# Optimization experiments

Hardware: AMD Instinct MI355X
Metric: run time of the kernel (lower is better)

## Reference

```python
import jax, jax.numpy as jnp
import numpy as np

B, T, D = 2, 2048, 2048
H, KV = 16, 4
HD = D // H  # 128
ROPE_BASE = 10000.0


def _rope(t):
    # t: [B, h, T, HD]; faithful to torch apply_rope (even/odd split, concat halves)
    pos = jnp.arange(T, dtype=t.dtype)
    inv_freq = 1.0 / (ROPE_BASE ** (jnp.arange(0, HD, 2, dtype=t.dtype) / HD))
    ang = jnp.einsum('t,f->tf', pos, inv_freq)  # [T, HD/2]
    sin = jnp.sin(ang)[None, None]
    cos = jnp.cos(ang)[None, None]
    t1, t2 = t[..., ::2], t[..., 1::2]
    return jnp.concatenate([t1 * cos - t2 * sin, t1 * sin + t2 * cos], axis=-1)


def setup_inputs() -> dict:
    key = jax.random.key(0)
    kx, kq, kk, kv, ko = jax.random.split(key, 5)
    x = jax.random.normal(kx, (B, T, D), dtype=jnp.float32)
    s = 0.02
    Wq = jax.random.normal(kq, (D, D), dtype=jnp.float32) * s
    Wk = jax.random.normal(kk, (D, KV * HD), dtype=jnp.float32) * s
    Wv = jax.random.normal(kv, (D, KV * HD), dtype=jnp.float32) * s
    Wo = jax.random.normal(ko, (D, D), dtype=jnp.float32) * s
    return {"x": x, "Wq": Wq, "Wk": Wk, "Wv": Wv, "Wo": Wo}


def reference(x, Wq, Wk, Wv, Wo):
    # projections (nn.Linear, no bias)
    q = (x @ Wq).reshape(B, T, H, HD).transpose(0, 2, 1, 3)    # [B,H,T,HD]
    k = (x @ Wk).reshape(B, T, KV, HD).transpose(0, 2, 1, 3)   # [B,KV,T,HD]
    v = (x @ Wv).reshape(B, T, KV, HD).transpose(0, 2, 1, 3)
    q = _rope(q)
    k = _rope(k)
    # GQA: repeat_interleave kv heads to full head count
    g = H // KV
    k = jnp.repeat(k, g, axis=1)
    v = jnp.repeat(v, g, axis=1)
    # causal SDPA, default scale 1/sqrt(head_dim)
    scale = 1.0 / jnp.sqrt(jnp.array(HD, dtype=x.dtype))
    scores = jnp.einsum('bhqd,bhkd->bhqk', q, k) * scale
    mask = jnp.tril(jnp.ones((T, T), dtype=bool))
    scores = jnp.where(mask, scores, jnp.finfo(scores.dtype).min)
    attn = jax.nn.softmax(scores, axis=-1)
    out = jnp.einsum('bhqk,bhkd->bhqd', attn, v)               # [B,H,T,HD]
    out = out.transpose(0, 2, 1, 3).reshape(B, T, D)
    return out @ Wo
```

## Files before the change

kernel.cpp:

```cpp
#include <hip/hip_runtime.h>
#include <math.h>

#define BB 2
#define TT 2048
#define DD 2048
#define HH 16
#define KVHN 4
#define HDIM 128
#define NKV 3072

typedef unsigned short u16;
typedef unsigned int u32;
typedef __bf16 bf16x8 __attribute__((ext_vector_type(8)));
typedef float  f32x4  __attribute__((ext_vector_type(4)));

#define AS1 __attribute__((address_space(1)))
#define AS3 __attribute__((address_space(3)))

__device__ __forceinline__ void dma16(const u16* g, u16* l) {
  __builtin_amdgcn_global_load_lds((const AS1 u32*)g, (AS3 u32*)l, 16, 0, 0);
}

__device__ __forceinline__ u16 f2bf(float f) {
  u32 u = __float_as_uint(f);
  u32 r = (u + 0x7FFFu + ((u >> 16) & 1u)) >> 16;
  return (u16)r;
}
__device__ __forceinline__ float bf2f(u32 h) { return __uint_as_float(h << 16); }

__device__ __forceinline__ u32 pack2(float a, float b) {
  union { __bf16 h[2]; u32 u; } cv;
  cv.h[0] = (__bf16)a; cv.h[1] = (__bf16)b;
  return cv.u;
}

__global__ __launch_bounds__(256) void castf2b(const float* __restrict__ in,
                                               u16* __restrict__ out) {
  size_t i4 = (size_t)blockIdx.x * 256 + threadIdx.x;
  float4 v = *(const float4*)(in + i4 * 4);
  ushort4 o;
  o.x = f2bf(v.x); o.y = f2bf(v.y); o.z = f2bf(v.z); o.w = f2bf(v.w);
  *(ushort4*)(out + i4 * 4) = o;
}

__global__ __launch_bounds__(256) void tcast(const float* __restrict__ W,
                                             u16* __restrict__ WT,
                                             int K, int N) {
  __shared__ float tile[32][33];
  const int n0 = blockIdx.x * 32, k0 = blockIdx.y * 32;
  const int r = threadIdx.x >> 3;
  const int c4 = (threadIdx.x & 7) * 4;
  float4 v = *(const float4*)(W + (size_t)(k0 + r) * N + n0 + c4);
  tile[r][c4 + 0] = v.x; tile[r][c4 + 1] = v.y;
  tile[r][c4 + 2] = v.z; tile[r][c4 + 3] = v.w;
  __syncthreads();
  ushort4 o;
  o.x = f2bf(tile[c4 + 0][r]); o.y = f2bf(tile[c4 + 1][r]);
  o.z = f2bf(tile[c4 + 2][r]); o.w = f2bf(tile[c4 + 3][r]);
  *(ushort4*)(WT + (size_t)(n0 + r) * K + k0 + c4) = o;
}

template <int OUT_BF16>
__global__ __launch_bounds__(512) void gemm8p(const u16* __restrict__ A,
                                              const u16* __restrict__ BT,
                                              void* __restrict__ Cv,
                                              int N, int K) {
  __shared__ u16 lds[3 * 24576];
  const int t = threadIdx.x;
  const int l = t & 63, w = t >> 6;
  const int lm = l & 15, quad = l >> 4;
  const int wm = w & 1, wn = w >> 1;
  const int m0 = blockIdx.y * 128, n0 = blockIdx.x * 256;
  const int wu = __builtin_amdgcn_readfirstlane(w);

  const u16* srcA[2]; int dstA[2];
  const u16* srcB[4]; int dstB[4];
  #pragma unroll
  for (int i = 0; i < 2; ++i) {
    int p0 = (wu * 2 + i) * 64, p = p0 + l;
    int row = p >> 3, c = (p & 7) ^ (row & 7);
    srcA[i] = A + (size_t)(m0 + row) * K + c * 8;
    dstA[i] = p0 * 8;
  }
  #pragma unroll
  for (int i = 0; i < 4; ++i) {
    int p0 = (wu * 4 + i) * 64, p = p0 + l;
    int row = p >> 3, c = (p & 7) ^ (row & 7);
    srcB[i] = BT + (size_t)(n0 + row) * K + c * 8;
    dstB[i] = 8192 + p0 * 8;
  }

  f32x4 acc[4][4];
  #pragma unroll
  for (int i = 0; i < 4; ++i)
    #pragma unroll
    for (int j = 0; j < 4; ++j) acc[i][j] = (f32x4){0.f, 0.f, 0.f, 0.f};

  auto stage = [&](int bsel) {
    u16* buf = &lds[bsel * 24576];
    #pragma unroll
    for (int i = 0; i < 2; ++i) { dma16(srcA[i], buf + dstA[i]); srcA[i] += 64; }
    #pragma unroll
    for (int i = 0; i < 4; ++i) { dma16(srcB[i], buf + dstB[i]); srcB[i] += 64; }
  };

  stage(0); stage(1); stage(2);

  const int NT = K >> 6;
  int bsel = 0;
  const int xorc = lm & 7;
  for (int tI = 0; tI < NT; ++tI) {
    if (tI + 2 < NT)      asm volatile("s_waitcnt vmcnt(12)" ::: "memory");
    else if (tI + 1 < NT) asm volatile("s_waitcnt vmcnt(6)" ::: "memory");
    else                  asm volatile("s_waitcnt vmcnt(0)" ::: "memory");
    asm volatile("s_barrier" ::: "memory");

    const u16* Ab = &lds[bsel * 24576];
    const u16* Bb = Ab + 8192;
    bf16x8 a[2][4], b[2][4];
    #pragma unroll
    for (int ks = 0; ks < 2; ++ks) {
      int ch = ((ks * 4 + quad) ^ xorc) * 8;
      #pragma unroll
      for (int i = 0; i < 4; ++i)
        a[ks][i] = *(const bf16x8*)&Ab[(wm * 64 + i * 16 + lm) * 64 + ch];
      #pragma unroll
      for (int j = 0; j < 4; ++j)
        b[ks][j] = *(const bf16x8*)&Bb[(wn * 64 + j * 16 + lm) * 64 + ch];
    }
    __builtin_amdgcn_s_setprio(1);
    #pragma unroll
    for (int ks = 0; ks < 2; ++ks)
      #pragma unroll
      for (int i = 0; i < 4; ++i)
        #pragma unroll
        for (int j = 0; j < 4; ++j)
          acc[i][j] = __builtin_amdgcn_mfma_f32_16x16x32_bf16(a[ks][i], b[ks][j], acc[i][j], 0, 0, 0);
    __builtin_amdgcn_s_setprio(0);
    asm volatile("s_barrier" ::: "memory");
    if (tI + 3 < NT) stage(bsel);
    bsel = (bsel == 2) ? 0 : bsel + 1;
  }

  #pragma unroll
  for (int i = 0; i < 4; ++i) {
    #pragma unroll
    for (int r = 0; r < 4; ++r) {
      size_t gr = (size_t)(m0 + wm * 64 + i * 16 + quad * 4 + r);
      #pragma unroll
      for (int j = 0; j < 4; ++j) {
        int gc = n0 + wn * 64 + j * 16 + lm;
        if (OUT_BF16) ((u16*)Cv)[gr * N + gc] = f2bf(acc[i][j][r]);
        else          ((float*)Cv)[gr * N + gc] = acc[i][j][r];
      }
    }
  }
}

__global__ __launch_bounds__(256) void rope2(u16* p) {
  const int row = blockIdx.x;
  const int pos = row & (TT - 1);
  u16* base = p + (size_t)row * NKV;
  float e0[5], e1[5];
  #pragma unroll
  for (int i = 0; i < 5; ++i) {
    int item = threadIdx.x + i * 256;
    int h20 = item >> 6, f = item & 63;
    int col = (h20 < 16) ? h20 * 128 : 2048 + (h20 - 16) * 128;
    u32 u = *(const u32*)(base + col + 2 * f);
    e0[i] = bf2f(u & 0xffffu);
    e1[i] = bf2f(u >> 16);
  }
  __syncthreads();
  #pragma unroll
  for (int i = 0; i < 5; ++i) {
    int item = threadIdx.x + i * 256;
    int h20 = item >> 6, f = item & 63;
    int col = (h20 < 16) ? h20 * 128 : 2048 + (h20 - 16) * 128;
    float sc = (h20 < 16) ? 0.08838834764831845f : 1.0f;
    float inv = exp2f((float)f * -0.20762050593046898f);
    float ang = (float)pos * inv;
    float sn, cs;
    sincosf(ang, &sn, &cs);
    base[col + f]      = f2bf((e0[i] * cs - e1[i] * sn) * sc);
    base[col + 64 + f] = f2bf((e0[i] * sn + e1[i] * cs) * sc);
  }
}

__global__ __launch_bounds__(256) void vtrans(const u16* __restrict__ QKV,
                                              u16* __restrict__ Vt) {
  __shared__ u16 tl[64][72];
  const int t0 = blockIdx.x * 64;
  const int y  = blockIdx.y;
  const int b  = blockIdx.z;
  #pragma unroll
  for (int i = 0; i < 2; ++i) {
    int idx = threadIdx.x + i * 256;
    int r = idx >> 3, c = (idx & 7) * 8;
    *(uint4*)&tl[r][c] =
        *(const uint4*)(QKV + (size_t)(b * TT + t0 + r) * NKV + 2560 + y * 64 + c);
  }
  __syncthreads();
  const int vh = y >> 1;
  #pragma unroll
  for (int i = 0; i < 2; ++i) {
    int idx = threadIdx.x + i * 256;
    int dr = idx >> 3, tc = (idx & 7) * 8;
    u16 tmp[8];
    #pragma unroll
    for (int j = 0; j < 8; ++j) tmp[j] = tl[tc + j][dr];
    int dloc = (y & 1) * 64 + dr;
    *(uint4*)(Vt + (size_t)((b * KVHN + vh) * HDIM + dloc) * TT + t0 + tc) =
        *(const uint4*)tmp;
  }
}

__global__ __launch_bounds__(256, 4) void attn4(const u16* __restrict__ QKV,
                                                const u16* __restrict__ Vt,
                                                u16* __restrict__ Ob) {
  __shared__ u16 KsA[32 * 128], KsB[32 * 128];
  __shared__ u16 VsA[64 * 64], VsB[64 * 64];
  __shared__ u16 Pw[4 * 512];
  const int t = threadIdx.x;
  const int l = t & 63, w = t >> 6;
  const int lm = l & 15, quad = l >> 4;
  const int h = blockIdx.y, b = blockIdx.z;
  const int qbase = (blockIdx.x + (blockIdx.y & 7)) & 31;
  const int qt = (blockIdx.y & 8) ? (31 - qbase) : qbase;
  const int kvh = h >> 2;
  const int q0 = qt * 64;
  const int last = 2 * qt + 1;
  const int wu = __builtin_amdgcn_readfirstlane(w);
  u16* pwv = &Pw[w * 512];
  constexpr float L2E = 1.4426950408889634f;

  bf16x8 qf[4];
  {
    size_t r0 = (size_t)(b * TT + q0 + w * 16 + lm) * NKV + h * HDIM;
    #pragma unroll
    for (int ks = 0; ks < 4; ++ks)
      qf[ks] = *(const bf16x8*)(QKV + r0 + ks * 32 + quad * 8);
  }

  f32x4 o[8];
  #pragma unroll
  for (int i = 0; i < 8; ++i) o[i] = (f32x4){0.f, 0.f, 0.f, 0.f};
  float m_ = -1e30f, l_ = 0.f;

  const u16 *kg[2], *vg[2];
  int koff[2], voff[2];
  #pragma unroll
  for (int i = 0; i < 2; ++i) {
    int p0 = (wu * 2 + i) * 64, p = p0 + l;
    int krow = p >> 4, kcp = p & 15, kcl = kcp ^ (krow & 15);
    kg[i] = QKV + (size_t)(b * TT + krow) * NKV + 2048 + kvh * HDIM + kcl * 8;
    koff[i] = p0 * 8;
    int vrow = p >> 3, vphys = p & 7, vcl = vphys ^ (vrow & 7);
    int vd = vrow + (vcl >> 2) * 64, vtch = vcl & 3;
    vg[i] = Vt + (size_t)((b * KVHN + kvh) * HDIM + vd) * TT + vtch * 8;
    voff[i] = p0 * 8;
  }

  #pragma unroll
  for (int i = 0; i < 2; ++i) {
    dma16(kg[i], KsA + koff[i]);
    dma16(vg[i], VsA + voff[i]);
    kg[i] += 32 * NKV;
    vg[i] += 32;
  }

  const int qrow = q0 + w * 16 + lm;

  auto body = [&](int kt, const u16* kcur, const u16* vcur, u16* knx, u16* vnx) {
    __syncthreads();
    const bool pf = kt < last;
    if (pf) {
      #pragma unroll
      for (int i = 0; i < 2; ++i) dma16(vg[i], vnx + voff[i]);
    }

    f32x4 s[2];
    s[0] = (f32x4){0.f, 0.f, 0.f, 0.f};
    s[1] = (f32x4){0.f, 0.f, 0.f, 0.f};
    __builtin_amdgcn_s_setprio(1);
    #pragma unroll
    for (int ks = 0; ks < 4; ++ks) {
      #pragma unroll
      for (int mt = 0; mt < 2; ++mt) {
        bf16x8 kb = *(const bf16x8*)&kcur[(mt * 16 + lm) * 128 + (((ks * 4 + quad) ^ lm) * 8)];
        s[mt] = __builtin_amdgcn_mfma_f32_16x16x32_bf16(kb, qf[ks], s[mt], 0, 0, 0);
      }
    }
    __builtin_amdgcn_s_setprio(0);
    if (pf) {
      #pragma unroll
      for (int i = 0; i < 2; ++i) {
        dma16(kg[i], knx + koff[i]);
        kg[i] += 32 * NKV;
        vg[i] += 32;
      }
    }

    if (kt >= 2 * qt) {
      #pragma unroll
      for (int mt = 0; mt < 2; ++mt)
        #pragma unroll
        for (int r = 0; r < 4; ++r) {
          int kv = kt * 32 + mt * 16 + quad * 4 + r;
          if (kv > qrow) s[mt][r] = -1e30f;
        }
    }

    float mx = -1e30f;
    #pragma unroll
    for (int mt = 0; mt < 2; ++mt)
      #pragma unroll
      for (int r = 0; r < 4; ++r) mx = fmaxf(mx, s[mt][r]);
    mx = fmaxf(mx, __shfl_xor(mx, 16));
    mx = fmaxf(mx, __shfl_xor(mx, 32));
    bool upd = mx > m_ + 8.f;
    float mn = upd ? mx : m_;
    float al = upd ? exp2f((m_ - mn) * L2E) : 1.f;
    m_ = mn;
    float sum = 0.f;
    #pragma unroll
    for (int mt = 0; mt < 2; ++mt)
      #pragma unroll
      for (int r = 0; r < 4; ++r) {
        float pv = exp2f((s[mt][r] - mn) * L2E);
        s[mt][r] = pv;
        sum += pv;
      }
    sum += __shfl_xor(sum, 16);
    sum += __shfl_xor(sum, 32);
    l_ = l_ * al + sum;

    #pragma unroll
    for (int mt = 0; mt < 2; ++mt) {
      u32 p01 = pack2(s[mt][0], s[mt][1]);
      u32 p23 = pack2(s[mt][2], s[mt][3]);
      int c = mt * 2 + (quad >> 1);
      int addr = (lm >> 1) * 64 + ((lm & 1) * 4 + (c ^ ((lm >> 1) & 3))) * 8 + (quad & 1) * 4;
      uint2 uv; uv.x = p01; uv.y = p23;
      *(uint2*)&pwv[addr] = uv;
    }
    if (__any(upd)) {
      #pragma unroll
      for (int i = 0; i < 8; ++i)
        #pragma unroll
        for (int r = 0; r < 4; ++r) o[i][r] *= al;
    }

    int paddr = (lm >> 1) * 64 + ((lm & 1) * 4 + (quad ^ ((lm >> 1) & 3))) * 8;
    bf16x8 pb = *(const bf16x8*)&pwv[paddr];
    __builtin_amdgcn_s_setprio(1);
    #pragma unroll
    for (int mt2 = 0; mt2 < 8; ++mt2) {
      int vrow = (mt2 & 3) * 16 + lm;
      int vphys = ((mt2 >> 2) * 4 + quad) ^ (vrow & 7);
      bf16x8 vb = *(const bf16x8*)&vcur[vrow * 64 + vphys * 8];
      o[mt2] = __builtin_amdgcn_mfma_f32_16x16x32_bf16(vb, pb, o[mt2], 0, 0, 0);
    }
    __builtin_amdgcn_s_setprio(0);
  };

  for (int kt = 0; kt <= last; ++kt) {
    if ((kt & 1) == 0) body(kt, KsA, VsA, KsB, VsB);
    else               body(kt, KsB, VsB, KsA, VsA);
  }

  __syncthreads();
  u16* esc = ((w & 2) ? KsB : KsA) + (w & 1) * 2048;
  float inv = 1.f / l_;
  #pragma unroll
  for (int mt2 = 0; mt2 < 8; ++mt2) {
    u32 a0 = pack2(o[mt2][0] * inv, o[mt2][1] * inv);
    u32 a1 = pack2(o[mt2][2] * inv, o[mt2][3] * inv);
    int phys = (mt2 * 2 + (quad >> 1)) ^ (lm & 7);
    int addr = lm * 128 + phys * 8 + (quad & 1) * 4;
    uint2 uv; uv.x = a0; uv.y = a1;
    *(uint2*)&esc[addr] = uv;
  }
  #pragma unroll
  for (int i = 0; i < 4; ++i) {
    int p = i * 64 + l;
    int row = p >> 4, cl = p & 15;
    int cph = cl ^ (row & 7);
    uint4 val = *(const uint4*)&esc[row * 128 + cph * 8];
    *(uint4*)(Ob + (size_t)(b * TT + q0 + w * 16 + row) * DD + h * HDIM + cl * 8) = val;
  }
}

extern "C" void kernel_launch(void* const* d_in, const int* in_sizes, int n_in,
                              void* d_out, int out_size, void* d_ws, size_t ws_size,
                              hipStream_t stream) {
  const float* x  = (const float*)d_in[0];
  const float* Wq = (const float*)d_in[1];
  const float* Wk = (const float*)d_in[2];
  const float* Wv = (const float*)d_in[3];
  const float* Wo = (const float*)d_in[4];
  float* out = (float*)d_out;

  u16* xb    = (u16*)d_ws;
  u16* WqkvT = xb + 8388608;
  u16* WoT   = xb + 14680064;
  u16* Vt    = WqkvT;
  u16* Ob    = xb;
  u16* QKVb  = (u16*)d_out;

  dim3 blk(256);
  castf2b<<<8192, blk, 0, stream>>>(x, xb);
  tcast<<<dim3(64, 64), blk, 0, stream>>>(Wq, WqkvT, DD, DD);
  tcast<<<dim3(16, 64), blk, 0, stream>>>(Wk, WqkvT + (size_t)2048 * DD, DD, 512);
  tcast<<<dim3(16, 64), blk, 0, stream>>>(Wv, WqkvT + (size_t)2560 * DD, DD, 512);
  tcast<<<dim3(64, 64), blk, 0, stream>>>(Wo, WoT, DD, DD);

  gemm8p<1><<<dim3(NKV / 256, 32), dim3(512), 0, stream>>>(xb, WqkvT, QKVb, NKV, DD);
  rope2<<<BB * TT, blk, 0, stream>>>(QKVb);
  vtrans<<<dim3(32, 8, BB), blk, 0, stream>>>(QKVb, Vt);
  attn4<<<dim3(32, HH, BB), blk, 0, stream>>>(QKVb, Vt, Ob);
  gemm8p<0><<<dim3(DD / 256, 32), dim3(512), 0, stream>>>(Ob, WoT, out, DD, DD);
}
```

Baseline: 326.4 us.

## Halve GEMM K-tile to 32 and triple-buffer attention K/V loads

The GEMM now stages 32-wide K tiles instead of 64, with the swizzle and vmcnt thresholds adjusted. This halves LDS per block, which may allow more resident blocks, but doubles the number of barrier iterations. The attention kernel replaces its double buffer with a three-stage K/V ring that uses explicit vmcnt waits and two barriers per iteration, and its launch bound drops to 3 waves. The aim is deeper prefetch to hide load latency, at the cost of more LDS and lower target occupancy.

```diff
diff --git a/kernel.cpp b/kernel.cpp
--- a/kernel.cpp
+++ b/kernel.cpp
@@ -65,7 +65,7 @@
                                               const u16* __restrict__ BT,
                                               void* __restrict__ Cv,
                                               int N, int K) {
-  __shared__ u16 lds[3 * 24576];
+  __shared__ u16 lds[3 * 12288];
   const int t = threadIdx.x;
   const int l = t & 63, w = t >> 6;
   const int lm = l & 15, quad = l >> 4;
@@ -73,21 +73,20 @@
   const int m0 = blockIdx.y * 128, n0 = blockIdx.x * 256;
   const int wu = __builtin_amdgcn_readfirstlane(w);
 
-  const u16* srcA[2]; int dstA[2];
-  const u16* srcB[4]; int dstB[4];
+  const u16* srcA; int dstA;
+  const u16* srcB[2]; int dstB[2];
+  {
+    int p0 = wu * 64, p = p0 + l;
+    int row = p >> 2, c = (p & 3) ^ (row & 3);
+    srcA = A + (size_t)(m0 + row) * K + c * 8;
+    dstA = p0 * 8;
+  }
   #pragma unroll
   for (int i = 0; i < 2; ++i) {
     int p0 = (wu * 2 + i) * 64, p = p0 + l;
-    int row = p >> 3, c = (p & 7) ^ (row & 7);
-    srcA[i] = A + (size_t)(m0 + row) * K + c * 8;
-    dstA[i] = p0 * 8;
-  }
-  #pragma unroll
-  for (int i = 0; i < 4; ++i) {
-    int p0 = (wu * 4 + i) * 64, p = p0 + l;
-    int row = p >> 3, c = (p & 7) ^ (row & 7);
+    int row = p >> 2, c = (p & 3) ^ (row & 3);
     srcB[i] = BT + (size_t)(n0 + row) * K + c * 8;
-    dstB[i] = 8192 + p0 * 8;
+    dstB[i] = 4096 + p0 * 8;
   }
 
   f32x4 acc[4][4];
@@ -97,45 +96,39 @@
     for (int j = 0; j < 4; ++j) acc[i][j] = (f32x4){0.f, 0.f, 0.f, 0.f};
 
   auto stage = [&](int bsel) {
-    u16* buf = &lds[bsel * 24576];
-    #pragma unroll
-    for (int i = 0; i < 2; ++i) { dma16(srcA[i], buf + dstA[i]); srcA[i] += 64; }
-    #pragma unroll
-    for (int i = 0; i < 4; ++i) { dma16(srcB[i], buf + dstB[i]); srcB[i] += 64; }
+    u16* buf = &lds[bsel * 12288];
+    dma16(srcA, buf + dstA); srcA += 32;
+    #pragma unroll
+    for (int i = 0; i < 2; ++i) { dma16(srcB[i], buf + dstB[i]); srcB[i] += 32; }
   };
 
   stage(0); stage(1); stage(2);
 
-  const int NT = K >> 6;
+  const int NT = K >> 5;
   int bsel = 0;
-  const int xorc = lm & 7;
+  const int xc = lm & 3;
   for (int tI = 0; tI < NT; ++tI) {
-    if (tI + 2 < NT)      asm volatile("s_waitcnt vmcnt(12)" ::: "memory");
-    else if (tI + 1 < NT) asm volatile("s_waitcnt vmcnt(6)" ::: "memory");
+    if (tI + 2 < NT)      asm volatile("s_waitcnt vmcnt(6)" ::: "memory");
+    else if (tI + 1 < NT) asm volatile("s_waitcnt vmcnt(3)" ::: "memory");
     else                  asm volatile("s_waitcnt vmcnt(0)" ::: "memory");
     asm volatile("s_barrier" ::: "memory");
 
-    const u16* Ab = &lds[bsel * 24576];
-    const u16* Bb = Ab + 8192;
-    bf16x8 a[2][4], b[2][4];
-    #pragma unroll
-    for (int ks = 0; ks < 2; ++ks) {
-      int ch = ((ks * 4 + quad) ^ xorc) * 8;
-      #pragma unroll
-      for (int i = 0; i < 4; ++i)
-        a[ks][i] = *(const bf16x8*)&Ab[(wm * 64 + i * 16 + lm) * 64 + ch];
+    const u16* Ab = &lds[bsel * 12288];
+    const u16* Bb = Ab + 4096;
+    const int ch = (quad ^ xc) * 8;
+    bf16x8 a[4], b[4];
+    #pragma unroll
+    for (int i = 0; i < 4; ++i)
+      a[i] = *(const bf16x8*)&Ab[(wm * 64 + i * 16 + lm) * 32 + ch];
+    #pragma unroll
+    for (int j = 0; j < 4; ++j)
+      b[j] = *(const bf16x8*)&Bb[(wn * 64 + j * 16 + lm) * 32 + ch];
+    __builtin_amdgcn_s_setprio(1);
+    #pragma unroll
+    for (int i = 0; i < 4; ++i)
       #pragma unroll
       for (int j = 0; j < 4; ++j)
-        b[ks][j] = *(const bf16x8*)&Bb[(wn * 64 + j * 16 + lm) * 64 + ch];
-    }
-    __builtin_amdgcn_s_setprio(1);
-    #pragma unroll
-    for (int ks = 0; ks < 2; ++ks)
-      #pragma unroll
-      for (int i = 0; i < 4; ++i)
-        #pragma unroll
-        for (int j = 0; j < 4; ++j)
-          acc[i][j] = __builtin_amdgcn_mfma_f32_16x16x32_bf16(a[ks][i], b[ks][j], acc[i][j], 0, 0, 0);
+        acc[i][j] = __builtin_amdgcn_mfma_f32_16x16x32_bf16(a[i], b[j], acc[i][j], 0, 0, 0);
     __builtin_amdgcn_s_setprio(0);
     asm volatile("s_barrier" ::: "memory");
     if (tI + 3 < NT) stage(bsel);
@@ -215,11 +208,11 @@
   }
 }
 
-__global__ __launch_bounds__(256, 4) void attn4(const u16* __restrict__ QKV,
+__global__ __launch_bounds__(256, 3) void attn5(const u16* __restrict__ QKV,
                                                 const u16* __restrict__ Vt,
                                                 u16* __restrict__ Ob) {
-  __shared__ u16 KsA[32 * 128], KsB[32 * 128];
-  __shared__ u16 VsA[64 * 64], VsB[64 * 64];
+  __shared__ u16 Ks[3 * 4096];
+  __shared__ u16 Vs[3 * 4096];
   __shared__ u16 Pw[4 * 512];
   const int t = threadIdx.x;
   const int l = t & 63, w = t >> 6;
@@ -261,23 +254,31 @@
     voff[i] = p0 * 8;
   }
 
-  #pragma unroll
-  for (int i = 0; i < 2; ++i) {
-    dma16(kg[i], KsA + koff[i]);
-    dma16(vg[i], VsA + voff[i]);
-    kg[i] += 32 * NKV;
-    vg[i] += 32;
-  }
+  auto stageKV = [&](int bsel) {
+    u16* kd = Ks + bsel * 4096;
+    u16* vd = Vs + bsel * 4096;
+    #pragma unroll
+    for (int i = 0; i < 2; ++i) {
+      dma16(kg[i], kd + koff[i]);  kg[i] += 32 * NKV;
+      dma16(vg[i], vd + voff[i]);  vg[i] += 32;
+    }
+  };
+
+  stageKV(0);
+  if (1 <= last) stageKV(1);
+  if (2 <= last) stageKV(2);
 
   const int qrow = q0 + w * 16 + lm;
 
-  auto body = [&](int kt, const u16* kcur, const u16* vcur, u16* knx, u16* vnx) {
-    __syncthreads();
-    const bool pf = kt < last;
-    if (pf) {
-      #pragma unroll
-      for (int i = 0; i < 2; ++i) dma16(vg[i], vnx + voff[i]);
-    }
+  int bs = 0;
+  for (int kt = 0; kt <= last; ++kt) {
+    if (kt + 2 <= last)      asm volatile("s_waitcnt vmcnt(8)" ::: "memory");
+    else if (kt + 1 <= last) asm volatile("s_waitcnt vmcnt(4)" ::: "memory");
+    else                     asm volatile("s_waitcnt vmcnt(0)" ::: "memory");
+    asm volatile("s_barrier" ::: "memory");
+
+    const u16* kcur = Ks + bs * 4096;
+    const u16* vcur = Vs + bs * 4096;
 
     f32x4 s[2];
     s[0] = (f32x4){0.f, 0.f, 0.f, 0.f};
@@ -292,14 +293,6 @@
       }
     }
     __builtin_amdgcn_s_setprio(0);
-    if (pf) {
-      #pragma unroll
-      for (int i = 0; i < 2; ++i) {
-        dma16(kg[i], knx + koff[i]);
-        kg[i] += 32 * NKV;
-        vg[i] += 32;
-      }
-    }
 
     if (kt >= 2 * qt) {
       #pragma unroll
@@ -362,15 +355,14 @@
       o[mt2] = __builtin_amdgcn_mfma_f32_16x16x32_bf16(vb, pb, o[mt2], 0, 0, 0);
     }
     __builtin_amdgcn_s_setprio(0);
-  };
-
-  for (int kt = 0; kt <= last; ++kt) {
-    if ((kt & 1) == 0) body(kt, KsA, VsA, KsB, VsB);
-    else               body(kt, KsB, VsB, KsA, VsA);
+
+    asm volatile("s_barrier" ::: "memory");
+    if (kt + 3 <= last) stageKV(bs);
+    bs = (bs == 2) ? 0 : bs + 1;
   }
 
   __syncthreads();
-  u16* esc = ((w & 2) ? KsB : KsA) + (w & 1) * 2048;
+  u16* esc = Ks + (w >> 1) * 4096 + (w & 1) * 2048;
   float inv = 1.f / l_;
   #pragma unroll
   for (int mt2 = 0; mt2 < 8; ++mt2) {
@@ -418,6 +410,6 @@
   gemm8p<1><<<dim3(NKV / 256, 32), dim3(512), 0, stream>>>(xb, WqkvT, QKVb, NKV, DD);
   rope2<<<BB * TT, blk, 0, stream>>>(QKVb);
   vtrans<<<dim3(32, 8, BB), blk, 0, stream>>>(QKVb, Vt);
-  attn4<<<dim3(32, HH, BB), blk, 0, stream>>>(QKVb, Vt, Ob);
+  attn5<<<dim3(32, HH, BB), blk, 0, stream>>>(QKVb, Vt, Ob);
   gemm8p<0><<<dim3(DD / 256, 32), dim3(512), 0, stream>>>(Ob, WoT, out, DD, DD);
 }
```

After: 341.3 us. +4.6%, slower.

## Interleave next-tile DMA with MFMA phases in GEMM, prefetch depth two

Applied to the files above, without the earlier changes.

Restructures the GEMM main loop so the global-to-LDS loads for the tile two steps ahead are issued in two halves between the k-sub-step LDS reads, each followed by a barrier and its MFMA batch. Previously a whole tile was staged only after all MFMAs finished. Prefetch depth drops from three tiles in flight to two, with matching waitcnt values. Lane-to-address mapping for the DMA becomes thread-contiguous. The aim is to spread memory issue across compute and cut post-compute stalls, at the cost of extra barriers per tile and less latency hiding.

```diff
diff --git a/kernel.cpp b/kernel.cpp
--- a/kernel.cpp
+++ b/kernel.cpp
@@ -61,7 +61,7 @@
 }
 
 template <int OUT_BF16>
-__global__ __launch_bounds__(512) void gemm8p(const u16* __restrict__ A,
+__global__ __launch_bounds__(512) void gemm4p(const u16* __restrict__ A,
                                               const u16* __restrict__ BT,
                                               void* __restrict__ Cv,
                                               int N, int K) {
@@ -72,22 +72,23 @@
   const int wm = w & 1, wn = w >> 1;
   const int m0 = blockIdx.y * 128, n0 = blockIdx.x * 256;
   const int wu = __builtin_amdgcn_readfirstlane(w);
+  const int tid = wu * 64 + l;
 
   const u16* srcA[2]; int dstA[2];
   const u16* srcB[4]; int dstB[4];
   #pragma unroll
   for (int i = 0; i < 2; ++i) {
-    int p0 = (wu * 2 + i) * 64, p = p0 + l;
+    int p = tid + i * 512;
     int row = p >> 3, c = (p & 7) ^ (row & 7);
     srcA[i] = A + (size_t)(m0 + row) * K + c * 8;
-    dstA[i] = p0 * 8;
+    dstA[i] = p * 8;
   }
   #pragma unroll
   for (int i = 0; i < 4; ++i) {
-    int p0 = (wu * 4 + i) * 64, p = p0 + l;
+    int p = tid + i * 512;
     int row = p >> 3, c = (p & 7) ^ (row & 7);
     srcB[i] = BT + (size_t)(n0 + row) * K + c * 8;
-    dstB[i] = 8192 + p0 * 8;
+    dstB[i] = 8192 + p * 8;
   }
 
   f32x4 acc[4][4];
@@ -96,7 +97,7 @@
     #pragma unroll
     for (int j = 0; j < 4; ++j) acc[i][j] = (f32x4){0.f, 0.f, 0.f, 0.f};
 
-  auto stage = [&](int bsel) {
+  auto stage_full = [&](int bsel) {
     u16* buf = &lds[bsel * 24576];
     #pragma unroll
     for (int i = 0; i < 2; ++i) { dma16(srcA[i], buf + dstA[i]); srcA[i] += 64; }
@@ -104,42 +105,53 @@
     for (int i = 0; i < 4; ++i) { dma16(srcB[i], buf + dstB[i]); srcB[i] += 64; }
   };
 
-  stage(0); stage(1); stage(2);
+  stage_full(0); stage_full(1);
 
   const int NT = K >> 6;
-  int bsel = 0;
-  const int xorc = lm & 7;
   for (int tI = 0; tI < NT; ++tI) {
-    if (tI + 2 < NT)      asm volatile("s_waitcnt vmcnt(12)" ::: "memory");
-    else if (tI + 1 < NT) asm volatile("s_waitcnt vmcnt(6)" ::: "memory");
-    else                  asm volatile("s_waitcnt vmcnt(0)" ::: "memory");
+    if (tI + 1 < NT) asm volatile("s_waitcnt vmcnt(6)" ::: "memory");
+    else             asm volatile("s_waitcnt vmcnt(0)" ::: "memory");
     asm volatile("s_barrier" ::: "memory");
 
-    const u16* Ab = &lds[bsel * 24576];
+    const u16* Ab = &lds[(tI % 3) * 24576];
     const u16* Bb = Ab + 8192;
-    bf16x8 a[2][4], b[2][4];
+    u16* nbuf = &lds[((tI + 2) % 3) * 24576];
+    const bool st = (tI + 2) < NT;
+
     #pragma unroll
     for (int ks = 0; ks < 2; ++ks) {
-      int ch = ((ks * 4 + quad) ^ xorc) * 8;
-      #pragma unroll
-      for (int i = 0; i < 4; ++i)
-        a[ks][i] = *(const bf16x8*)&Ab[(wm * 64 + i * 16 + lm) * 64 + ch];
-      #pragma unroll
-      for (int j = 0; j < 4; ++j)
-        b[ks][j] = *(const bf16x8*)&Bb[(wn * 64 + j * 16 + lm) * 64 + ch];
-    }
-    __builtin_amdgcn_s_setprio(1);
-    #pragma unroll
-    for (int ks = 0; ks < 2; ++ks)
+      bf16x8 a[4], b[4];
+      #pragma unroll
+      for (int i = 0; i < 4; ++i) {
+        int row = wm * 64 + i * 16 + lm;
+        a[i] = *(const bf16x8*)&Ab[row * 64 + (((ks * 4 + quad) ^ (row & 7)) * 8)];
+      }
+      #pragma unroll
+      for (int j = 0; j < 4; ++j) {
+        int row = wn * 64 + j * 16 + lm;
+        b[j] = *(const bf16x8*)&Bb[row * 64 + (((ks * 4 + quad) ^ (row & 7)) * 8)];
+      }
+      if (st) {
+        if (ks == 0) {
+          dma16(srcA[0], nbuf + dstA[0]); srcA[0] += 64;
+          dma16(srcA[1], nbuf + dstA[1]); srcA[1] += 64;
+          dma16(srcB[0], nbuf + dstB[0]); srcB[0] += 64;
+        } else {
+          dma16(srcB[1], nbuf + dstB[1]); srcB[1] += 64;
+          dma16(srcB[2], nbuf + dstB[2]); srcB[2] += 64;
+          dma16(srcB[3], nbuf + dstB[3]); srcB[3] += 64;
+        }
+      }
+      asm volatile("s_barrier" ::: "memory");
+      __builtin_amdgcn_s_setprio(1);
       #pragma unroll
       for (int i = 0; i < 4; ++i)
         #pragma unroll
         for (int j = 0; j < 4; ++j)
-          acc[i][j] = __builtin_amdgcn_mfma_f32_16x16x32_bf16(a[ks][i], b[ks][j], acc[i][j], 0, 0, 0);
-    __builtin_amdgcn_s_setprio(0);
-    asm volatile("s_barrier" ::: "memory");
-    if (tI + 3 < NT) stage(bsel);
-    bsel = (bsel == 2) ? 0 : bsel + 1;
+          acc[i][j] = __builtin_amdgcn_mfma_f32_16x16x32_bf16(a[i], b[j], acc[i][j], 0, 0, 0);
+      __builtin_amdgcn_s_setprio(0);
+      asm volatile("s_barrier" ::: "memory");
+    }
   }
 
   #pragma unroll
@@ -415,9 +427,9 @@
   tcast<<<dim3(16, 64), blk, 0, stream>>>(Wv, WqkvT + (size_t)2560 * DD, DD, 512);
   tcast<<<dim3(64, 64), blk, 0, stream>>>(Wo, WoT, DD, DD);
 
-  gemm8p<1><<<dim3(NKV / 256, 32), dim3(512), 0, stream>>>(xb, WqkvT, QKVb, NKV, DD);
+  gemm4p<1><<<dim3(NKV / 256, 32), dim3(512), 0, stream>>>(xb, WqkvT, QKVb, NKV, DD);
   rope2<<<BB * TT, blk, 0, stream>>>(QKVb);
   vtrans<<<dim3(32, 8, BB), blk, 0, stream>>>(QKVb, Vt);
   attn4<<<dim3(32, HH, BB), blk, 0, stream>>>(QKVb, Vt, Ob);
-  gemm8p<0><<<dim3(DD / 256, 32), dim3(512), 0, stream>>>(Ob, WoT, out, DD, DD);
-}
+  gemm4p<0><<<dim3(DD / 256, 32), dim3(512), 0, stream>>>(Ob, WoT, out, DD, DD);
+}
```

Measured after the change: 337.8 us. 1.04x slower.
